# Kernel optimization log

Hardware: AMD Instinct MI355X
Metric: run time of the kernel (lower is better)

## Reference

```python
import jax, jax.numpy as jnp
import numpy as np

B, V, H, W = 8, 2, 1024, 1024
N = 131072
TH_MIN, TH_MAX = 0.0, 500.0
ALPHA = 0.5


def _make_extrinsics():
    # Random small-rotation camera-to-world poses (invertible 4x4), fixed seed.
    rng = np.random.default_rng(0)
    E = np.tile(np.eye(4, dtype=np.float32), (B, V, 1, 1))
    for bi in range(B):
        for vi in range(V):
            ang = rng.uniform(-0.15, 0.15)
            ax = rng.normal(size=3)
            ax = ax / np.linalg.norm(ax)
            K = np.array([[0.0, -ax[2], ax[1]], [ax[2], 0.0, -ax[0]], [-ax[1], ax[0], 0.0]])
            R = np.eye(3) + np.sin(ang) * K + (1.0 - np.cos(ang)) * (K @ K)
            E[bi, vi, :3, :3] = R.astype(np.float32)
            E[bi, vi, :3, 3] = (rng.normal(size=3) * 0.5).astype(np.float32)
    return jnp.asarray(E)


def setup_inputs():
    key = jax.random.key(0)
    k0, k1, k2, k3, k4 = jax.random.split(key, 5)
    scale = jnp.array([W - 1.0, H - 1.0], jnp.float32)
    mkpts0 = jax.random.uniform(k0, (N, 2), dtype=jnp.float32) * scale
    mkpts1 = jax.random.uniform(k1, (N, 2), dtype=jnp.float32) * scale
    mconf = jax.random.uniform(k2, (N,), jnp.float32, 0.2, 1.0)
    mbids = jnp.sort(jax.random.randint(k3, (N,), 0, B, dtype=jnp.int32))
    intr = jnp.tile(jnp.array([[1.0, 0.0, 0.5], [0.0, 1.0, 0.5], [0.0, 0.0, 1.0]], jnp.float32), (B, V, 1, 1))
    extr = _make_extrinsics()
    disps = jax.random.uniform(k4, (V * B, 1, H, W), jnp.float32, 0.01, 1.0)
    return {"mkpts0": mkpts0, "mkpts1": mkpts1, "mconf": mconf, "mbids": mbids,
            "intrinsics": intr, "extrinsics": extr, "fullres_disps": disps}


def _forward(mkpts0, mkpts1, mconf, mbids, intrinsics, extrinsics, fullres_disps):
    b, v = intrinsics.shape[:2]
    _, _, h, w = fullres_disps.shape
    # intr0[0,:]*=w ; intr0[1,:]*=h  (normalized -> pixel intrinsics)
    row_scale = jnp.array([float(w), float(h), 1.0], intrinsics.dtype)[None, None, :, None]
    intr = intrinsics * row_scale                                    # (b,v,3,3)
    extr_inv = jnp.linalg.inv(extrinsics)                            # (b,v,4,4)
    proj = jnp.einsum('bvij,bvjk->bvik', intr, extr_inv[:, :, :3, :])  # (b,v,3,4)

    # --- per-keypoint DLT triangulation (vectorized over all N matches) ---
    P = proj[mbids]                                                  # (N,v,3,4)
    pts2 = jnp.stack([mkpts0, mkpts1], axis=1)                       # (N,v,2)
    # rows: conf*(x*P[2]-P[0]), conf*(y*P[2]-P[1])
    A = P[:, :, 2:3, :] * pts2[..., None] - P[:, :, :2, :]           # (N,v,2,4)
    A = A * mconf[:, None, None, None]
    A = A.reshape(-1, 2 * v, 4)                                      # (N,4,4)
    _, _, vh = jnp.linalg.svd(A, full_matrices=False)
    hom = vh[:, -1, :]                                               # last right singular vector
    pts_world = hom[:, :3] / hom[:, 3:4]                             # (N,3)

    # transform into each camera frame: pc_transform(pts, extr.inverse())
    pw_h = jnp.concatenate([pts_world, jnp.ones_like(pts_world[:, :1])], axis=-1)
    pts_cam = jnp.einsum('nvij,nj->nvi', extr_inv[mbids], pw_h)[..., :3]  # (N,v,3)
    z = pts_cam[..., 2]                                              # (N,v)
    valid = jnp.all((z > TH_MIN) & (z < TH_MAX), axis=1)             # (N,)

    # --- near/far over valid matched depths per (scene, view) ---
    zmin = jnp.where(valid[:, None], z, jnp.inf)
    zmax = jnp.where(valid[:, None], z, -jnp.inf)
    near = jax.ops.segment_min(zmin, mbids, num_segments=b)          # (b,v)
    far = jax.ops.segment_max(zmax, mbids, num_segments=b)
    has = jax.ops.segment_max(valid.astype(jnp.float32), mbids, num_segments=b)
    flag = jnp.broadcast_to(has[:, None], (b, v))                    # (b,v)
    near = jnp.where(flag > 0, near, 0.0)
    far = jnp.where(flag > 0, far, 500.0)

    # --- fusion_mkpt_costvolum: scatter 1/z into the cost-volume disparities ---
    disps = fullres_disps.reshape(v, b, h, w)                        # '(v b) 1 h w'
    mk_x = jnp.clip(jnp.stack([mkpts0[:, 0], mkpts1[:, 0]], 1).astype(jnp.int32), 0, w - 1)  # (N,v)
    mk_y = jnp.clip(jnp.stack([mkpts0[:, 1], mkpts1[:, 1]], 1).astype(jnp.int32), 0, h - 1)
    mk_z = 1.0 / z                                                   # matched disparity (N,v)
    view_idx = jnp.broadcast_to(jnp.arange(v, dtype=jnp.int32)[None, :], mk_x.shape)
    bids2 = jnp.broadcast_to(mbids[:, None], mk_x.shape)
    cost = disps[view_idx, bids2, mk_y, mk_x]                        # gather existing disparity
    val = ALPHA * mk_z + (1.0 - ALPHA) * cost                        # alpha-weighted fusion
    val = jnp.where(valid[:, None], val, cost)                       # masked-out matches: no-op write
    disps = disps.at[view_idx, bids2, mk_y, mk_x].set(val)
    fused = disps.reshape(v * b, 1, h, w)
    return fused, near, far, flag


def reference(mkpts0, mkpts1, mconf, mbids, intrinsics, extrinsics, fullres_disps):
    return _forward(mkpts0, mkpts1, mconf, mbids, intrinsics, extrinsics, fullres_disps)
```

## Files before the change

### kernel.cpp

```cpp
#include <hip/hip_runtime.h>
#include <math.h>

#define BB 8
#define VV 2
#define HH 1024
#define WW 1024
#define NPTS 131072
#define IMG (HH*WW)
#define FUSED (VV*BB*IMG)

#define NSOLVE (NPTS/256)
#define NCLEAR ((2*NPTS)/256)
#define NCOPY  (FUSED/4/256)

typedef float f32x4 __attribute__((ext_vector_type(4)));

#define OFF_Z    0u
#define OFF_PIX  (8u*NPTS)
#define OFF_RED  (16u*NPTS)
#define OFF_WIN  (OFF_RED + 0x20000u)
#define WS_NEED  ((size_t)OFF_WIN + 4ull*(size_t)FUSED)

__device__ __forceinline__ int clampi(int v, int lo, int hi) {
    return v < lo ? lo : (v > hi ? hi : v);
}

__device__ __forceinline__ void prep_one(int t, const float* __restrict__ intr,
                                         const float* __restrict__ extr, double* sD) {
    const float* E = extr + t * 16;
    double R[3][3], tr[3];
#pragma unroll
    for (int i = 0; i < 3; i++) {
#pragma unroll
        for (int j = 0; j < 3; j++) R[i][j] = (double)E[i * 4 + j];
        tr[i] = (double)E[i * 4 + 3];
    }
    double inv[3][4];
#pragma unroll
    for (int i = 0; i < 3; i++) {
#pragma unroll
        for (int j = 0; j < 3; j++) inv[i][j] = R[j][i];
        inv[i][3] = -(R[0][i] * tr[0] + R[1][i] * tr[1] + R[2][i] * tr[2]);
    }
    const float* K = intr + t * 9;
    double rs[3] = {(double)WW, (double)HH, 1.0};
#pragma unroll
    for (int i = 0; i < 3; i++)
#pragma unroll
        for (int k = 0; k < 4; k++) {
            double s = 0.0;
#pragma unroll
            for (int j = 0; j < 3; j++) s += (double)K[i * 3 + j] * rs[i] * inv[j][k];
            sD[t * 12 + i * 4 + k] = s;
        }
#pragma unroll
    for (int k = 0; k < 4; k++) sD[192 + t * 4 + k] = inv[2][k];
}

template <int DEDUP>
__global__ __launch_bounds__(256) void mega_kernel(
        const f32x4* __restrict__ src, f32x4* __restrict__ dst,
        const float2* __restrict__ mk0, const float2* __restrict__ mk1,
        const int* __restrict__ mbids,
        const float* __restrict__ intr, const float* __restrict__ extr,
        const float* __restrict__ disps,
        float* __restrict__ out, char* __restrict__ ws) {
    int b = blockIdx.x, t = threadIdx.x;

    if (b >= NSOLVE + NCLEAR) {
        int i = (b - NSOLVE - NCLEAR) * 256 + t;
        f32x4 v = src[i];
        __builtin_nontemporal_store(v, &dst[i]);
        return;
    }
    if (b >= NSOLVE) {
        if (DEDUP) {
            int id = (b - NSOLVE) * 256 + t;
            int n = id >> 1, v = id & 1;
            const float2* mk = v ? mk1 : mk0;
            float2 q = mk[n];
            int xi = clampi((int)q.x, 0, WW - 1);
            int yi = clampi((int)q.y, 0, HH - 1);
            int bid = mbids[n];
            ((int*)(ws + OFF_WIN))[(v * BB + bid) * IMG + yi * WW + xi] = -1;
        }
        return;
    }

    __shared__ double sD[256];
    __shared__ int nearB[16], farB[16], hasB[8];
    if (t < 16) {
        prep_one(t, intr, extr, sD);
        nearB[t] = 0x7F800000;
        farB[t]  = 0;
        if (t < 8) hasB[t] = 0;
    }
    __syncthreads();

    int n = b * 256 + t;
    float* zarr   = (float*)(ws + OFF_Z);
    int*   pixarr = (int*)(ws + OFF_PIX);

    int bid = mbids[n];
    float2 q0 = mk0[n], q1 = mk1[n];
    float xf[2] = {q0.x, q1.x};
    float yf[2] = {q0.y, q1.y};

    double M[4][4];
#pragma unroll
    for (int i = 0; i < 4; i++)
#pragma unroll
        for (int j = 0; j < 4; j++) M[i][j] = 0.0;
#pragma unroll
    for (int v = 0; v < 2; v++) {
        const double* P = sD + (bid * VV + v) * 12;
        double xx = (double)xf[v], yy = (double)yf[v];
        double r0[4], r1[4];
#pragma unroll
        for (int j = 0; j < 4; j++) {
            r0[j] = xx * P[8 + j] - P[j];
            r1[j] = yy * P[8 + j] - P[4 + j];
        }
#pragma unroll
        for (int i = 0; i < 4; i++)
#pragma unroll
            for (int j = 0; j < 4; j++) M[i][j] += r0[i] * r0[j] + r1[i] * r1[j];
    }

    double Vm[4][4] = {{1, 0, 0, 0}, {0, 1, 0, 0}, {0, 0, 1, 0}, {0, 0, 0, 1}};
    for (int sweep = 0; sweep < 8; ++sweep) {
        double off = fabs(M[0][1]) + fabs(M[0][2]) + fabs(M[0][3]) +
                     fabs(M[1][2]) + fabs(M[1][3]) + fabs(M[2][3]);
        double dia = fabs(M[0][0]) + fabs(M[1][1]) + fabs(M[2][2]) + fabs(M[3][3]);
        if (off <= 1e-13 * dia) break;
#pragma unroll
        for (int p = 0; p < 3; p++) {
#pragma unroll
            for (int q = p + 1; q < 4; q++) {
                double apq = M[p][q];
                if (fabs(apq) < 1e-300) continue;
                double tau = (M[q][q] - M[p][p]) / (2.0 * apq);
                double rt  = sqrt(1.0 + tau * tau);
                double t_  = (tau >= 0.0) ? 1.0 / (tau + rt) : 1.0 / (tau - rt);
                double c = 1.0 / sqrt(1.0 + t_ * t_);
                double s = t_ * c;
#pragma unroll
                for (int k = 0; k < 4; k++) {
                    double mp = M[k][p], mq = M[k][q];
                    M[k][p] = c * mp - s * mq;
                    M[k][q] = s * mp + c * mq;
                }
#pragma unroll
                for (int k = 0; k < 4; k++) {
                    double mp = M[p][k], mq = M[q][k];
                    M[p][k] = c * mp - s * mq;
                    M[q][k] = s * mp + c * mq;
                }
#pragma unroll
                for (int k = 0; k < 4; k++) {
                    double vp = Vm[k][p], vq = Vm[k][q];
                    Vm[k][p] = c * vp - s * vq;
                    Vm[k][q] = s * vp + c * vq;
                }
            }
        }
    }
    int jmin = 0; double dmin = M[0][0];
    if (M[1][1] < dmin) { dmin = M[1][1]; jmin = 1; }
    if (M[2][2] < dmin) { dmin = M[2][2]; jmin = 2; }
    if (M[3][3] < dmin) { dmin = M[3][3]; jmin = 3; }

    double ev[4];
#pragma unroll
    for (int i = 0; i < 4; i++) {
        double a01 = (jmin == 0) ? Vm[i][0] : Vm[i][1];
        double a23 = (jmin == 2) ? Vm[i][2] : Vm[i][3];
        ev[i] = (jmin < 2) ? a01 : a23;
    }
    double iw  = 1.0 / ev[3];
    double pwx = ev[0] * iw, pwy = ev[1] * iw, pwz = ev[2] * iw;

    double z[2];
#pragma unroll
    for (int v = 0; v < 2; v++) {
        const double* e = sD + 192 + (bid * VV + v) * 4;
        z[v] = e[0] * pwx + e[1] * pwy + e[2] * pwz + e[3];
    }
    bool valid = (z[0] > 0.0) && (z[0] < 500.0) && (z[1] > 0.0) && (z[1] < 500.0);

    unsigned long long vb = __ballot(valid);
    int bidFirst = __shfl(bid, 0);
    int bidLast  = __shfl(bid, 63);
    if (bidFirst == bidLast) {
        if (vb != 0ULL) {
            float zn[2], zf[2];
#pragma unroll
            for (int v = 0; v < 2; v++) {
                zn[v] = valid ? (float)z[v] : INFINITY;
                zf[v] = valid ? (float)z[v] : -1.0f;
            }
#pragma unroll
            for (int off = 32; off > 0; off >>= 1) {
#pragma unroll
                for (int v = 0; v < 2; v++) {
                    zn[v] = fminf(zn[v], __shfl_down(zn[v], off));
                    zf[v] = fmaxf(zf[v], __shfl_down(zf[v], off));
                }
            }
            if ((t & 63) == 0) {
#pragma unroll
                for (int v = 0; v < 2; v++) {
                    atomicMin(&nearB[bid * VV + v], __float_as_int(zn[v]));
                    atomicMax(&farB[bid * VV + v],  __float_as_int(zf[v]));
                }
                atomicOr(&hasB[bid], 1);
            }
        }
    } else if (valid) {
#pragma unroll
        for (int v = 0; v < 2; v++) {
            int fb = __float_as_int((float)z[v]);
            atomicMin(&nearB[bid * VV + v], fb);
            atomicMax(&farB[bid * VV + v],  fb);
        }
        atomicOr(&hasB[bid], 1);
    }

#pragma unroll
    for (int v = 0; v < 2; v++) {
        int xi = clampi((int)xf[v], 0, WW - 1);
        int yi = clampi((int)yf[v], 0, HH - 1);
        int pix = (v * BB + bid) * IMG + yi * WW + xi;
        if (DEDUP) {
            zarr[2 * n + v]   = valid ? (float)z[v] : 0.0f;
            pixarr[2 * n + v] = pix;
        } else {
            float cost = disps[pix];
            float val = valid ? (float)(0.5 * (1.0 / z[v]) + 0.5 * (double)cost) : cost;
            out[pix] = val;
        }
    }

    __syncthreads();
    int* red = (int*)(ws + OFF_RED) + b * 40;
    if (t < 16) {
        red[t]      = nearB[t];
        red[16 + t] = farB[t];
        if (t < 8) red[32 + t] = hasB[t];
    }
}

__global__ __launch_bounds__(256) void vote_kernel(char* __restrict__ ws) {
    int id = blockIdx.x * 256 + threadIdx.x;
    const int* pixarr = (const int*)(ws + OFF_PIX);
    int* winner = (int*)(ws + OFF_WIN);
    atomicMax(winner + pixarr[id], id >> 1);
}

__global__ __launch_bounds__(256) void resolve_kernel(const float* __restrict__ disps,
                                                      float* __restrict__ out,
                                                      const char* __restrict__ ws,
                                                      int dedup) {
    int id = blockIdx.x * 256 + threadIdx.x;
    if (dedup) {
        const float* zarr   = (const float*)(ws + OFF_Z);
        const int*   pixarr = (const int*)(ws + OFF_PIX);
        const int*   winner = (const int*)(ws + OFF_WIN);
        int   pix = pixarr[id];
        float zf  = zarr[id];
        if (winner[pix] == (id >> 1) && zf > 0.0f) {
            float cost = disps[pix];
            out[pix] = (float)(0.5 * (1.0 / (double)zf) + 0.5 * (double)cost);
        }
    }
    if (blockIdx.x == 0) {
        __shared__ int redLds[40];
        int t = threadIdx.x;
        const int* red = (const int*)(ws + OFF_RED);
        int w = t >> 6, lane = t & 63;
        for (int c = w; c < 40; c += 4) {
            int acc = (c < 16) ? 0x7F800000 : 0;
            for (int s = lane; s < NSOLVE; s += 64) {
                int vv = red[s * 40 + c];
                acc = (c < 16) ? min(acc, vv) : (c < 32 ? max(acc, vv) : (acc | vv));
            }
#pragma unroll
            for (int off = 32; off > 0; off >>= 1) {
                int o = __shfl_down(acc, off);
                acc = (c < 16) ? min(acc, o) : (c < 32 ? max(acc, o) : (acc | o));
            }
            if (lane == 0) redLds[c] = acc;
        }
        __syncthreads();
        if (t < 16) {
            int hv = redLds[32 + (t >> 1)];
            out[FUSED + t]               = hv ? __int_as_float(redLds[t])      : 0.0f;
            out[FUSED + BB * VV + t]     = hv ? __int_as_float(redLds[16 + t]) : 500.0f;
            out[FUSED + 2 * BB * VV + t] = hv ? 1.0f : 0.0f;
        }
    }
}

extern "C" void kernel_launch(void* const* d_in, const int* in_sizes, int n_in,
                              void* d_out, int out_size, void* d_ws, size_t ws_size,
                              hipStream_t stream) {
    const float* mk0   = (const float*)d_in[0];
    const float* mk1   = (const float*)d_in[1];
    const int*   mbids = (const int*)d_in[3];
    const float* intr  = (const float*)d_in[4];
    const float* extr  = (const float*)d_in[5];
    const float* disps = (const float*)d_in[6];
    float* out = (float*)d_out;
    char*  ws  = (char*)d_ws;

    bool dedup = (ws_size >= WS_NEED);
    dim3 grid(NSOLVE + NCLEAR + NCOPY);

    if (dedup) {
        mega_kernel<1><<<grid, 256, 0, stream>>>(
            (const f32x4*)disps, (f32x4*)out, (const float2*)mk0, (const float2*)mk1,
            mbids, intr, extr, disps, out, ws);
        vote_kernel<<<NCLEAR, 256, 0, stream>>>(ws);
        resolve_kernel<<<NCLEAR, 256, 0, stream>>>(disps, out, ws, 1);
    } else {
        mega_kernel<0><<<grid, 256, 0, stream>>>(
            (const f32x4*)disps, (f32x4*)out, (const float2*)mk0, (const float2*)mk1,
            mbids, intr, extr, disps, out, ws);
        resolve_kernel<<<1, 256, 0, stream>>>(disps, out, ws, 0);
    }
}
```

Before: 185.7 us.

## Fold winner-clear into solver and vectorize vote/resolve over point pairs

Drops the separate clear blocks: the solver threads now zero the winner slot for their own pixels and store the precomputed fused value rather than z. Vote and resolve process both views per thread with int2/float2 loads and offset IDs, so the zeroed slot never matches a real writer. The resolve pass no longer re-reads the disparity gather, and the near/far reduction moves into the vote kernel. A cleared slot could race with another block's atomicMax, since clear and vote now happen in different kernels. Ordering is still preserved because the clear finishes in the solver kernel before vote runs.

```diff
diff --git a/kernel.cpp b/kernel.cpp
--- a/kernel.cpp
+++ b/kernel.cpp
@@ -10,12 +10,11 @@
 #define FUSED (VV*BB*IMG)
 
 #define NSOLVE (NPTS/256)
-#define NCLEAR ((2*NPTS)/256)
 #define NCOPY  (FUSED/4/256)
 
 typedef float f32x4 __attribute__((ext_vector_type(4)));
 
-#define OFF_Z    0u
+#define OFF_VAL  0u
 #define OFF_PIX  (8u*NPTS)
 #define OFF_RED  (16u*NPTS)
 #define OFF_WIN  (OFF_RED + 0x20000u)
@@ -67,23 +66,10 @@
         float* __restrict__ out, char* __restrict__ ws) {
     int b = blockIdx.x, t = threadIdx.x;
 
-    if (b >= NSOLVE + NCLEAR) {
-        int i = (b - NSOLVE - NCLEAR) * 256 + t;
+    if (b >= NSOLVE) {
+        int i = (b - NSOLVE) * 256 + t;
         f32x4 v = src[i];
         __builtin_nontemporal_store(v, &dst[i]);
-        return;
-    }
-    if (b >= NSOLVE) {
-        if (DEDUP) {
-            int id = (b - NSOLVE) * 256 + t;
-            int n = id >> 1, v = id & 1;
-            const float2* mk = v ? mk1 : mk0;
-            float2 q = mk[n];
-            int xi = clampi((int)q.x, 0, WW - 1);
-            int yi = clampi((int)q.y, 0, HH - 1);
-            int bid = mbids[n];
-            ((int*)(ws + OFF_WIN))[(v * BB + bid) * IMG + yi * WW + xi] = -1;
-        }
         return;
     }
 
@@ -98,8 +84,9 @@
     __syncthreads();
 
     int n = b * 256 + t;
-    float* zarr   = (float*)(ws + OFF_Z);
+    float* valarr = (float*)(ws + OFF_VAL);
     int*   pixarr = (int*)(ws + OFF_PIX);
+    int*   winner = (int*)(ws + OFF_WIN);
 
     int bid = mbids[n];
     float2 q0 = mk0[n], q1 = mk1[n];
@@ -231,11 +218,13 @@
         int xi = clampi((int)xf[v], 0, WW - 1);
         int yi = clampi((int)yf[v], 0, HH - 1);
         int pix = (v * BB + bid) * IMG + yi * WW + xi;
+        float cost = disps[pix];
         if (DEDUP) {
-            zarr[2 * n + v]   = valid ? (float)z[v] : 0.0f;
+            winner[pix] = 0;
+            valarr[2 * n + v] = valid ? (float)(0.5 * (1.0 / z[v]) + 0.5 * (double)cost)
+                                      : 0.0f;
             pixarr[2 * n + v] = pix;
         } else {
-            float cost = disps[pix];
             float val = valid ? (float)(0.5 * (1.0 / z[v]) + 0.5 * (double)cost) : cost;
             out[pix] = val;
         }
@@ -250,55 +239,60 @@
     }
 }
 
-__global__ __launch_bounds__(256) void vote_kernel(char* __restrict__ ws) {
-    int id = blockIdx.x * 256 + threadIdx.x;
-    const int* pixarr = (const int*)(ws + OFF_PIX);
+__device__ __forceinline__ void reduce_nearfar(const char* __restrict__ ws,
+                                               float* __restrict__ out) {
+    __shared__ int redLds[40];
+    int t = threadIdx.x;
+    const int* red = (const int*)(ws + OFF_RED);
+    int w = t >> 6, lane = t & 63;
+    for (int c = w; c < 40; c += 4) {
+        int acc = (c < 16) ? 0x7F800000 : 0;
+        for (int s = lane; s < NSOLVE; s += 64) {
+            int vv = red[s * 40 + c];
+            acc = (c < 16) ? min(acc, vv) : (c < 32 ? max(acc, vv) : (acc | vv));
+        }
+#pragma unroll
+        for (int off = 32; off > 0; off >>= 1) {
+            int o = __shfl_down(acc, off);
+            acc = (c < 16) ? min(acc, o) : (c < 32 ? max(acc, o) : (acc | o));
+        }
+        if (lane == 0) redLds[c] = acc;
+    }
+    __syncthreads();
+    if (t < 16) {
+        int hv = redLds[32 + (t >> 1)];
+        out[FUSED + t]               = hv ? __int_as_float(redLds[t])      : 0.0f;
+        out[FUSED + BB * VV + t]     = hv ? __int_as_float(redLds[16 + t]) : 500.0f;
+        out[FUSED + 2 * BB * VV + t] = hv ? 1.0f : 0.0f;
+    }
+}
+
+__global__ __launch_bounds__(256) void vote_kernel(char* __restrict__ ws,
+                                                   float* __restrict__ out) {
+    int gid = blockIdx.x * 256 + threadIdx.x;
+    const int2* pix2 = (const int2*)(ws + OFF_PIX);
     int* winner = (int*)(ws + OFF_WIN);
-    atomicMax(winner + pixarr[id], id >> 1);
-}
-
-__global__ __launch_bounds__(256) void resolve_kernel(const float* __restrict__ disps,
-                                                      float* __restrict__ out,
-                                                      const char* __restrict__ ws,
-                                                      int dedup) {
-    int id = blockIdx.x * 256 + threadIdx.x;
-    if (dedup) {
-        const float* zarr   = (const float*)(ws + OFF_Z);
-        const int*   pixarr = (const int*)(ws + OFF_PIX);
-        const int*   winner = (const int*)(ws + OFF_WIN);
-        int   pix = pixarr[id];
-        float zf  = zarr[id];
-        if (winner[pix] == (id >> 1) && zf > 0.0f) {
-            float cost = disps[pix];
-            out[pix] = (float)(0.5 * (1.0 / (double)zf) + 0.5 * (double)cost);
-        }
-    }
-    if (blockIdx.x == 0) {
-        __shared__ int redLds[40];
-        int t = threadIdx.x;
-        const int* red = (const int*)(ws + OFF_RED);
-        int w = t >> 6, lane = t & 63;
-        for (int c = w; c < 40; c += 4) {
-            int acc = (c < 16) ? 0x7F800000 : 0;
-            for (int s = lane; s < NSOLVE; s += 64) {
-                int vv = red[s * 40 + c];
-                acc = (c < 16) ? min(acc, vv) : (c < 32 ? max(acc, vv) : (acc | vv));
-            }
-#pragma unroll
-            for (int off = 32; off > 0; off >>= 1) {
-                int o = __shfl_down(acc, off);
-                acc = (c < 16) ? min(acc, o) : (c < 32 ? max(acc, o) : (acc | o));
-            }
-            if (lane == 0) redLds[c] = acc;
-        }
-        __syncthreads();
-        if (t < 16) {
-            int hv = redLds[32 + (t >> 1)];
-            out[FUSED + t]               = hv ? __int_as_float(redLds[t])      : 0.0f;
-            out[FUSED + BB * VV + t]     = hv ? __int_as_float(redLds[16 + t]) : 500.0f;
-            out[FUSED + 2 * BB * VV + t] = hv ? 1.0f : 0.0f;
-        }
-    }
+    int2 p = pix2[gid];
+    atomicMax(winner + p.x, 2 * gid + 1);
+    atomicMax(winner + p.y, 2 * gid + 2);
+    if (blockIdx.x == 0) reduce_nearfar(ws, out);
+}
+
+__global__ __launch_bounds__(256) void resolve_kernel(float* __restrict__ out,
+                                                      const char* __restrict__ ws) {
+    int gid = blockIdx.x * 256 + threadIdx.x;
+    const int2*   pix2 = (const int2*)(ws + OFF_PIX);
+    const float2* val2 = (const float2*)(ws + OFF_VAL);
+    const int*    winner = (const int*)(ws + OFF_WIN);
+    int2 p = pix2[gid];
+    float2 v = val2[gid];
+    if (v.x > 0.0f && winner[p.x] == 2 * gid + 1) out[p.x] = v.x;
+    if (v.y > 0.0f && winner[p.y] == 2 * gid + 2) out[p.y] = v.y;
+}
+
+__global__ __launch_bounds__(256) void reduce_kernel(float* __restrict__ out,
+                                                     const char* __restrict__ ws) {
+    reduce_nearfar(ws, out);
 }
 
 extern "C" void kernel_launch(void* const* d_in, const int* in_sizes, int n_in,
@@ -314,18 +308,18 @@
     char*  ws  = (char*)d_ws;
 
     bool dedup = (ws_size >= WS_NEED);
-    dim3 grid(NSOLVE + NCLEAR + NCOPY);
+    dim3 grid(NSOLVE + NCOPY);
 
     if (dedup) {
         mega_kernel<1><<<grid, 256, 0, stream>>>(
             (const f32x4*)disps, (f32x4*)out, (const float2*)mk0, (const float2*)mk1,
             mbids, intr, extr, disps, out, ws);
-        vote_kernel<<<NCLEAR, 256, 0, stream>>>(ws);
-        resolve_kernel<<<NCLEAR, 256, 0, stream>>>(disps, out, ws, 1);
+        vote_kernel<<<NSOLVE, 256, 0, stream>>>(ws, out);
+        resolve_kernel<<<NSOLVE, 256, 0, stream>>>(out, ws);
     } else {
         mega_kernel<0><<<grid, 256, 0, stream>>>(
             (const f32x4*)disps, (f32x4*)out, (const float2*)mk0, (const float2*)mk1,
             mbids, intr, extr, disps, out, ws);
-        resolve_kernel<<<1, 256, 0, stream>>>(disps, out, ws, 0);
-    }
-}
+        reduce_kernel<<<1, 256, 0, stream>>>(out, ws);
+    }
+}
```

Result: no change. 184.0 us (-0.9%).
